# Kernel tuning notes

Hardware: AMD Instinct MI355X
Metric: run time of the kernel (lower is better)

The kernel has to match this reference:

```python
import jax, jax.numpy as jnp
import numpy as np

BATCH, INPUT_DIM, HIDDEN_DIM, SEQ_LENGTH = 128, 256, 512, 1024


def setup_inputs() -> dict:
    key = jax.random.key(0)
    k1, k2, k3, k4, k5 = jax.random.split(key, 5)
    s = 1.0 / np.sqrt(HIDDEN_DIM)  # PyTorch GRU init: U(-1/sqrt(H), 1/sqrt(H))
    return {
        "input_features": jax.random.normal(k1, (BATCH, INPUT_DIM), dtype=jnp.float32),
        # PyTorch layout: rows stacked as [reset; update; new], each [H, *]
        "w_ih": jax.random.uniform(k2, (3 * HIDDEN_DIM, INPUT_DIM), minval=-s, maxval=s, dtype=jnp.float32),
        "w_hh": jax.random.uniform(k3, (3 * HIDDEN_DIM, HIDDEN_DIM), minval=-s, maxval=s, dtype=jnp.float32),
        "b_ih": jax.random.uniform(k4, (3 * HIDDEN_DIM,), minval=-s, maxval=s, dtype=jnp.float32),
        "b_hh": jax.random.uniform(k5, (3 * HIDDEN_DIM,), minval=-s, maxval=s, dtype=jnp.float32),
    }


def reference(input_features, w_ih, w_hh, b_ih, b_hh):
    # Decoder: run the GRU cell SEQ_LENGTH times with the SAME input x each
    # step, feeding back the hidden state; collect per-step outputs.
    B = input_features.shape[0]
    H = w_hh.shape[1]
    # Input contribution is constant across steps -> compute once.  [B, 3H]
    gi = input_features @ w_ih.T + b_ih
    gi_r, gi_z, gi_n = jnp.split(gi, 3, axis=-1)

    def step(h, _):
        gh = h @ w_hh.T + b_hh  # [B, 3H]
        gh_r, gh_z, gh_n = jnp.split(gh, 3, axis=-1)
        r = jax.nn.sigmoid(gi_r + gh_r)
        z = jax.nn.sigmoid(gi_z + gh_z)
        n = jnp.tanh(gi_n + r * gh_n)
        h_new = (1.0 - z) * n + z * h
        return h_new, h_new

    h0 = jnp.zeros((B, H), dtype=input_features.dtype)
    _, outs = jax.lax.scan(step, h0, None, length=SEQ_LENGTH)  # [S, B, H]
    return jnp.transpose(outs, (1, 0, 2))  # [B, SEQ_LENGTH, H]
```

## Files before the change

### kernel.cpp

```cpp
#include <hip/hip_runtime.h>
#include <hip/hip_bf16.h>
#include <stdint.h>


constexpr int SEQ = 1024;
constexpr int BATCH = 128;
constexpr int IND = 256;
constexpr int HD = 512;
constexpr int BG = 8;
constexpr int HG = 32;
constexpr int ROWS = BATCH / BG;
constexpr int NT = 3;

using frag16 = __attribute__((ext_vector_type(8))) short;
using f32x4  = __attribute__((ext_vector_type(4))) float;

constexpr size_t HX_BUF_ULL = (size_t)BG * 2048;
constexpr size_t WS_FLAGS   = 2 * HX_BUF_ULL * 8;

__device__ __forceinline__ float sigmoid_f(float x) {
    return 1.f / (1.f + __expf(-x));
}
__device__ __forceinline__ float tanh_f(float x) {
    float e = __expf(2.f * x);
    return 1.f - 2.f / (e + 1.f);
}
__device__ __forceinline__ unsigned short f2bfu(float x) {
    return __bfloat16_as_ushort(__float2bfloat16(x));
}

__global__ __launch_bounds__(64) void gru_kernel(
    const float* __restrict__ x,
    const float* __restrict__ w_ih,
    const float* __restrict__ w_hh,
    const float* __restrict__ b_ih,
    const float* __restrict__ b_hh,
    unsigned long long* __restrict__ hx,
    unsigned* __restrict__ flags,
    float* __restrict__ out)
{
    const int lane = threadIdx.x;
    const int bg = blockIdx.x & 7;
    const int hg = blockIdx.x >> 3;
    const int b0 = bg * ROWS;
    const int c0 = hg * 16;
    const int nlo = lane & 15;
    const int quad = lane >> 4;

    int gcol[NT];
    gcol[0] = c0 + nlo;
    gcol[1] = HD + c0 + nlo;
    gcol[2] = 2 * HD + c0 + nlo;

    __shared__ frag16 ldsB[NT * 16 * 64];
#pragma unroll
    for (int t = 0; t < NT; ++t) {
        for (int kc = 0; kc < 16; ++kc) {
            const float* src = w_hh + (size_t)gcol[t] * HD + kc * 32 + quad * 8;
            float4 v0 = *(const float4*)src;
            float4 v1 = *(const float4*)(src + 4);
            frag16 f;
            f[0] = (short)f2bfu(v0.x); f[1] = (short)f2bfu(v0.y);
            f[2] = (short)f2bfu(v0.z); f[3] = (short)f2bfu(v0.w);
            f[4] = (short)f2bfu(v1.x); f[5] = (short)f2bfu(v1.y);
            f[6] = (short)f2bfu(v1.z); f[7] = (short)f2bfu(v1.w);
            ldsB[(t * 16 + kc) * 64 + lane] = f;
        }
    }

    float gi[NT][4];
    float bhn = b_hh[gcol[2]];
#pragma unroll
    for (int t = 0; t < NT; ++t) {
        float bi = b_ih[gcol[t]] + ((t < 2) ? b_hh[gcol[t]] : 0.f);
#pragma unroll
        for (int r = 0; r < 4; ++r) gi[t][r] = bi;
    }
    for (int r = 0; r < 4; ++r) {
        const float4* xr = (const float4*)(x + (size_t)(b0 + quad * 4 + r) * IND);
        for (int kc = 0; kc < IND / 4; ++kc) {
            float4 xv = xr[kc];
#pragma unroll
            for (int t = 0; t < NT; ++t) {
                float4 wv = ((const float4*)(w_ih + (size_t)gcol[t] * IND))[kc];
                gi[t][r] += xv.x * wv.x + xv.y * wv.y + xv.z * wv.z + xv.w * wv.w;
            }
        }
    }

    float hreg[4];
#pragma unroll
    for (int r = 0; r < 4; ++r) hreg[r] = 0.f;

    unsigned* myflag = flags + bg * HG + hg;
    unsigned* pollflag = flags + bg * HG + (lane & 31);

    for (int s = 0; s < SEQ; ++s) {
        f32x4 C[NT];
#pragma unroll
        for (int t = 0; t < NT; ++t) C[t] = (f32x4){0.f, 0.f, 0.f, 0.f};

        if (s > 0) {
            const unsigned long long* hb =
                hx + ((size_t)(s & 1) * BG + bg) * 2048 + (size_t)lane * 2;
            unsigned long long a0[16], a1[16];
#pragma unroll
            for (int kc = 0; kc < 16; ++kc) {
                a0[kc] = __hip_atomic_load(hb + kc * 128,     __ATOMIC_RELAXED, __HIP_MEMORY_SCOPE_SYSTEM);
                a1[kc] = __hip_atomic_load(hb + kc * 128 + 1, __ATOMIC_RELAXED, __HIP_MEMORY_SCOPE_SYSTEM);
            }
#pragma unroll
            for (int kc = 0; kc < 16; ++kc) {
                union { unsigned long long u[2]; frag16 f; } af;
                af.u[0] = a0[kc];
                af.u[1] = a1[kc];
#pragma unroll
                for (int t = 0; t < NT; ++t) {
                    frag16 bfr = ldsB[(t * 16 + kc) * 64 + lane];
                    C[t] = __builtin_amdgcn_mfma_f32_16x16x32_bf16(af.f, bfr, C[t], 0, 0, 0);
                }
            }
        }

        unsigned long long* hw = hx + ((size_t)((s + 1) & 1) * BG + bg) * 2048;
        float ov[4];
#pragma unroll
        for (int r = 0; r < 4; ++r) {
            float gr  = gi[0][r] + C[0][r];
            float gz  = gi[1][r] + C[1][r];
            float ghn = C[2][r] + bhn;
            float rr = sigmoid_f(gr);
            float zz = sigmoid_f(gz);
            float nn = tanh_f(gi[2][r] + rr * ghn);
            float hn = (1.f - zz) * nn + zz * hreg[r];
            hreg[r] = hn;
            ov[r] = hn;
            unsigned own = (unsigned)f2bfu(hn);
            unsigned v0 = own | ((unsigned)__shfl_xor((int)own, 1) << 16);
            unsigned w1 = (unsigned)__shfl_xor((int)v0, 2);
            unsigned u2 = (unsigned)__shfl_xor((int)v0, 4);
            unsigned u3 = (unsigned)__shfl_xor((int)w1, 4);
            if ((lane & 7) == 0) {
                unsigned long long lo = (unsigned long long)v0 | ((unsigned long long)w1 << 32);
                unsigned long long hi = (unsigned long long)u2 | ((unsigned long long)u3 << 32);
                size_t ci = (size_t)hg * 64 + (size_t)(nlo >> 3) * 32 + (size_t)(quad * 4 + r) * 2;
                __hip_atomic_store(hw + ci,     lo, __ATOMIC_RELAXED, __HIP_MEMORY_SCOPE_SYSTEM);
                __hip_atomic_store(hw + ci + 1, hi, __ATOMIC_RELAXED, __HIP_MEMORY_SCOPE_SYSTEM);
            }
        }

        if (s < SEQ - 1) {
            asm volatile("s_waitcnt vmcnt(0)" ::: "memory");
            if (lane == 0)
                __hip_atomic_store(myflag, (unsigned)(s + 1),
                                   __ATOMIC_RELAXED, __HIP_MEMORY_SCOPE_SYSTEM);
            asm volatile("" ::: "memory");
        }

        {
            float* op = out + (size_t)(b0 + quad * 4) * (SEQ * HD) + (size_t)s * HD + c0 + nlo;
#pragma unroll
            for (int r = 0; r < 4; ++r)
                op[(size_t)r * (SEQ * HD)] = ov[r];
        }

        if (s < SEQ - 1) {
            asm volatile("" ::: "memory");
            bool done = false;
            do {
                unsigned v = __hip_atomic_load(pollflag, __ATOMIC_RELAXED,
                                               __HIP_MEMORY_SCOPE_SYSTEM);
                done = (__ballot(v > (unsigned)s) == ~0ull);
            } while (!done);
            asm volatile("" ::: "memory");
        }
    }
}

extern "C" void kernel_launch(void* const* d_in, const int* in_sizes, int n_in,
                              void* d_out, int out_size, void* d_ws, size_t ws_size,
                              hipStream_t stream) {
    (void)in_sizes; (void)n_in; (void)out_size; (void)ws_size;
    const float* x    = (const float*)d_in[0];
    const float* w_ih = (const float*)d_in[1];
    const float* w_hh = (const float*)d_in[2];
    const float* b_ih = (const float*)d_in[3];
    const float* b_hh = (const float*)d_in[4];

    char* ws = (char*)d_ws;
    unsigned long long* hx = (unsigned long long*)ws;
    unsigned* flags = (unsigned*)(ws + WS_FLAGS);

    hipMemsetAsync(flags, 0, (size_t)BG * HG * sizeof(unsigned), stream);
    gru_kernel<<<BG * HG, 64, 0, stream>>>(x, w_ih, w_hh, b_ih, b_hh, hx, flags,
                                           (float*)d_out);
}
```

Measured before the change: 3.461 ms.

## Replace flag barrier with tag bits embedded in hidden-state data ring

Removes the per-step flag store and the flag polling barrier. Instead, a step tag is written into the low mantissa bit of each bf16 hidden value, and consumers spin on the data itself. The hidden-state exchange becomes an 8-deep buffer ring, and each 32-wide K chunk is fed to MFMA as soon as its tag matches, overlapping partial arrivals with compute. This cuts a global round-trip per step at the cost of one bit of bf16 precision in h. It also relies on tags never matching stale workspace contents, since the workspace is no longer cleared.

```diff
diff --git a/kernel.cpp b/kernel.cpp
--- a/kernel.cpp
+++ b/kernel.cpp
@@ -11,12 +11,12 @@
 constexpr int HG = 32;
 constexpr int ROWS = BATCH / BG;
 constexpr int NT = 3;
+constexpr int NBUF = 8;
 
 using frag16 = __attribute__((ext_vector_type(8))) short;
 using f32x4  = __attribute__((ext_vector_type(4))) float;
 
-constexpr size_t HX_BUF_ULL = (size_t)BG * 2048;
-constexpr size_t WS_FLAGS   = 2 * HX_BUF_ULL * 8;
+constexpr unsigned long long TAGM = 0x0001000100010001ull;
 
 __device__ __forceinline__ float sigmoid_f(float x) {
     return 1.f / (1.f + __expf(-x));
@@ -27,6 +27,16 @@
 }
 __device__ __forceinline__ unsigned short f2bfu(float x) {
     return __bfloat16_as_ushort(__float2bfloat16(x));
+}
+__device__ __forceinline__ unsigned tag_of(unsigned long long a) {
+    unsigned lo = (unsigned)a, hi = (unsigned)(a >> 32);
+    return (lo & 1u) | ((lo >> 15) & 2u) | ((hi & 1u) << 2) | ((hi >> 13) & 8u);
+}
+__device__ __forceinline__ unsigned long long tag_pat(unsigned t) {
+    return (unsigned long long)(t & 1u)
+         | ((unsigned long long)((t >> 1) & 1u) << 16)
+         | ((unsigned long long)((t >> 2) & 1u) << 32)
+         | ((unsigned long long)((t >> 3) & 1u) << 48);
 }
 
 __global__ __launch_bounds__(64) void gru_kernel(
@@ -36,7 +46,6 @@
     const float* __restrict__ b_ih,
     const float* __restrict__ b_hh,
     unsigned long long* __restrict__ hx,
-    unsigned* __restrict__ flags,
     float* __restrict__ out)
 {
     const int lane = threadIdx.x;
@@ -92,9 +101,6 @@
 #pragma unroll
     for (int r = 0; r < 4; ++r) hreg[r] = 0.f;
 
-    unsigned* myflag = flags + bg * HG + hg;
-    unsigned* pollflag = flags + bg * HG + (lane & 31);
-
     for (int s = 0; s < SEQ; ++s) {
         f32x4 C[NT];
 #pragma unroll
@@ -102,27 +108,52 @@
 
         if (s > 0) {
             const unsigned long long* hb =
-                hx + ((size_t)(s & 1) * BG + bg) * 2048 + (size_t)lane * 2;
+                hx + ((size_t)(s & (NBUF - 1)) * BG + bg) * 2048 + (size_t)lane * 2;
+            const unsigned expect = (unsigned)(s % 15) + 1u;
             unsigned long long a0[16], a1[16];
+            unsigned valid = 0;
 #pragma unroll
             for (int kc = 0; kc < 16; ++kc) {
                 a0[kc] = __hip_atomic_load(hb + kc * 128,     __ATOMIC_RELAXED, __HIP_MEMORY_SCOPE_SYSTEM);
                 a1[kc] = __hip_atomic_load(hb + kc * 128 + 1, __ATOMIC_RELAXED, __HIP_MEMORY_SCOPE_SYSTEM);
             }
-#pragma unroll
-            for (int kc = 0; kc < 16; ++kc) {
-                union { unsigned long long u[2]; frag16 f; } af;
-                af.u[0] = a0[kc];
-                af.u[1] = a1[kc];
-#pragma unroll
-                for (int t = 0; t < NT; ++t) {
-                    frag16 bfr = ldsB[(t * 16 + kc) * 64 + lane];
-                    C[t] = __builtin_amdgcn_mfma_f32_16x16x32_bf16(af.f, bfr, C[t], 0, 0, 0);
+            while (true) {
+                unsigned newly = 0;
+#pragma unroll
+                for (int kc = 0; kc < 16; ++kc) {
+                    if (!(valid & (1u << kc))) {
+                        bool ok = (tag_of(a0[kc]) == expect) && (tag_of(a1[kc]) == expect);
+                        if (__ballot(ok) == ~0ull) newly |= 1u << kc;
+                    }
                 }
-            }
-        }
-
-        unsigned long long* hw = hx + ((size_t)((s + 1) & 1) * BG + bg) * 2048;
+#pragma unroll
+                for (int kc = 0; kc < 16; ++kc) {
+                    if (newly & (1u << kc)) {
+                        union { unsigned long long u[2]; frag16 f; } af;
+                        af.u[0] = a0[kc];
+                        af.u[1] = a1[kc];
+#pragma unroll
+                        for (int t = 0; t < NT; ++t) {
+                            frag16 bfr = ldsB[(t * 16 + kc) * 64 + lane];
+                            C[t] = __builtin_amdgcn_mfma_f32_16x16x32_bf16(af.f, bfr, C[t], 0, 0, 0);
+                        }
+                    }
+                }
+                valid |= newly;
+                if (valid == 0xFFFFu) break;
+#pragma unroll
+                for (int kc = 0; kc < 16; ++kc) {
+                    if (!(valid & (1u << kc))) {
+                        a0[kc] = __hip_atomic_load(hb + kc * 128,     __ATOMIC_RELAXED, __HIP_MEMORY_SCOPE_SYSTEM);
+                        a1[kc] = __hip_atomic_load(hb + kc * 128 + 1, __ATOMIC_RELAXED, __HIP_MEMORY_SCOPE_SYSTEM);
+                    }
+                }
+            }
+        }
+
+        unsigned long long* hw =
+            hx + ((size_t)((s + 1) & (NBUF - 1)) * BG + bg) * 2048;
+        const unsigned long long pat = tag_pat((unsigned)((s + 1) % 15) + 1u);
         float ov[4];
 #pragma unroll
         for (int r = 0; r < 4; ++r) {
@@ -143,36 +174,19 @@
             if ((lane & 7) == 0) {
                 unsigned long long lo = (unsigned long long)v0 | ((unsigned long long)w1 << 32);
                 unsigned long long hi = (unsigned long long)u2 | ((unsigned long long)u3 << 32);
+                lo = (lo & ~TAGM) | pat;
+                hi = (hi & ~TAGM) | pat;
                 size_t ci = (size_t)hg * 64 + (size_t)(nlo >> 3) * 32 + (size_t)(quad * 4 + r) * 2;
                 __hip_atomic_store(hw + ci,     lo, __ATOMIC_RELAXED, __HIP_MEMORY_SCOPE_SYSTEM);
                 __hip_atomic_store(hw + ci + 1, hi, __ATOMIC_RELAXED, __HIP_MEMORY_SCOPE_SYSTEM);
             }
         }
 
-        if (s < SEQ - 1) {
-            asm volatile("s_waitcnt vmcnt(0)" ::: "memory");
-            if (lane == 0)
-                __hip_atomic_store(myflag, (unsigned)(s + 1),
-                                   __ATOMIC_RELAXED, __HIP_MEMORY_SCOPE_SYSTEM);
-            asm volatile("" ::: "memory");
-        }
-
         {
             float* op = out + (size_t)(b0 + quad * 4) * (SEQ * HD) + (size_t)s * HD + c0 + nlo;
 #pragma unroll
             for (int r = 0; r < 4; ++r)
                 op[(size_t)r * (SEQ * HD)] = ov[r];
-        }
-
-        if (s < SEQ - 1) {
-            asm volatile("" ::: "memory");
-            bool done = false;
-            do {
-                unsigned v = __hip_atomic_load(pollflag, __ATOMIC_RELAXED,
-                                               __HIP_MEMORY_SCOPE_SYSTEM);
-                done = (__ballot(v > (unsigned)s) == ~0ull);
-            } while (!done);
-            asm volatile("" ::: "memory");
         }
     }
 }
@@ -187,11 +201,8 @@
     const float* b_ih = (const float*)d_in[3];
     const float* b_hh = (const float*)d_in[4];
 
-    char* ws = (char*)d_ws;
-    unsigned long long* hx = (unsigned long long*)ws;
-    unsigned* flags = (unsigned*)(ws + WS_FLAGS);
-
-    hipMemsetAsync(flags, 0, (size_t)BG * HG * sizeof(unsigned), stream);
-    gru_kernel<<<BG * HG, 64, 0, stream>>>(x, w_ih, w_hh, b_ih, b_hh, hx, flags,
+    unsigned long long* hx = (unsigned long long*)d_ws;
+
+    gru_kernel<<<BG * HG, 64, 0, stream>>>(x, w_ih, w_hh, b_ih, b_hh, hx,
                                            (float*)d_out);
 }
```

New measurement: 7.815 ms. 126% more time.
